# Kernel tuning notes

Measured on AMD Instinct MI355X. Metric: run time of the kernel, lower is better.

Reference implementation:

```python
import jax, jax.numpy as jnp
import numpy as np

B, H, W, C = 16, 64, 64, 512
WS, SS, NH = 8, 4, 16
HD = C // NH
N = WS * WS          # tokens per window = 64
NWH, NWW = H // WS, W // WS
NW = NWH * NWW       # windows per image = 64
HID = 2048
EPS = 1e-5

def _rel_pos_index():
    coords = np.stack(np.meshgrid(np.arange(WS), np.arange(WS), indexing='ij'))  # [2,ws,ws]
    cf = coords.reshape(2, -1)                      # [2,N]
    rel = cf[:, :, None] - cf[:, None, :]           # [2,N,N]
    rel = rel.transpose(1, 2, 0).astype(np.int64)   # [N,N,2]
    rel[:, :, 0] += WS - 1
    rel[:, :, 1] += WS - 1
    rel[:, :, 0] *= 2 * WS - 1
    return rel.sum(-1)                              # [N,N]

def _attn_mask():
    img = np.zeros((H, W), dtype=np.float32)
    cnt = 0
    sls = (slice(0, -WS), slice(-WS, -SS), slice(-SS, None))
    for hs in sls:
        for ws_ in sls:
            img[hs, ws_] = cnt
            cnt += 1
    mw = img.reshape(NWH, WS, NWW, WS).transpose(0, 2, 1, 3).reshape(-1, N)  # [nW,N]
    am = mw[:, None, :] - mw[:, :, None]            # [nW,N,N] (unsqueeze(1)-unsqueeze(2))
    return np.where(am != 0, np.float32(-100.0), np.float32(0.0))

_RPI = jnp.asarray(_rel_pos_index())
_AMASK = jnp.asarray(_attn_mask())

def _ln(x, g, b):
    m = jnp.mean(x, -1, keepdims=True)
    v = jnp.mean((x - m) ** 2, -1, keepdims=True)
    return (x - m) * jax.lax.rsqrt(v + EPS) * g + b

def setup_inputs() -> dict:
    key = jax.random.key(0)
    ks = jax.random.split(key, 8)
    s = 0.02
    return {
        'x': jax.random.normal(ks[0], (B, H * W, C), jnp.float32),
        'g1': jnp.ones((C,), jnp.float32), 'b1': jnp.zeros((C,), jnp.float32),
        'qkv_w': jax.random.normal(ks[1], (C, 3 * C), jnp.float32) * s,
        'qkv_b': jnp.zeros((3 * C,), jnp.float32),
        'proj_w': jax.random.normal(ks[2], (C, C), jnp.float32) * s,
        'proj_b': jnp.zeros((C,), jnp.float32),
        'rpb': jax.random.normal(ks[3], ((2 * WS - 1) ** 2, NH), jnp.float32) * s,
        'g2': jnp.ones((C,), jnp.float32), 'b2': jnp.zeros((C,), jnp.float32),
        'fc1_w': jax.random.normal(ks[4], (C, HID), jnp.float32) * s,
        'fc1_b': jnp.zeros((HID,), jnp.float32),
        'fc2_w': jax.random.normal(ks[5], (HID, C), jnp.float32) * s,
        'fc2_b': jnp.zeros((C,), jnp.float32),
    }

def reference(x, g1, b1, qkv_w, qkv_b, proj_w, proj_b, rpb, g2, b2, fc1_w, fc1_b, fc2_w, fc2_b):
    shortcut = x                                    # [B,L,C]
    xn = _ln(x, g1, b1).reshape(B, H, W, C)
    xs = jnp.roll(xn, (-SS, -SS), axis=(1, 2))      # cyclic shift
    # window partition -> [B*nW, N, C]
    xw = xs.reshape(B, NWH, WS, NWW, WS, C).transpose(0, 1, 3, 2, 4, 5).reshape(-1, N, C)
    # attention
    qkv = xw @ qkv_w + qkv_b                        # [Bw,N,3C]
    qkv = qkv.reshape(-1, N, 3, NH, HD).transpose(2, 0, 3, 1, 4)  # [3,Bw,NH,N,HD]
    q, k, v = qkv[0], qkv[1], qkv[2]
    scale = jnp.asarray(HD ** -0.5, xw.dtype)
    attn = jnp.einsum('bhnd,bhmd->bhnm', q, k) * scale            # [Bw,NH,N,N]
    bias = rpb[_RPI.reshape(-1)].reshape(N, N, NH).transpose(2, 0, 1)
    attn = attn + bias[None]
    attn = attn.reshape(B, NW, NH, N, N) + _AMASK[None, :, None]
    attn = jax.nn.softmax(attn.reshape(-1, NH, N, N), axis=-1)
    out = jnp.einsum('bhnm,bhmd->bhnd', attn, v)    # [Bw,NH,N,HD]
    out = out.transpose(0, 2, 1, 3).reshape(-1, N, C)
    out = out @ proj_w + proj_b
    # window reverse -> [B,H,W,C]
    xr = out.reshape(B, NWH, NWW, WS, WS, C).transpose(0, 1, 3, 2, 4, 5).reshape(B, H, W, C)
    xr = jnp.roll(xr, (SS, SS), axis=(1, 2)).reshape(B, H * W, C)
    x = shortcut + xr
    h = _ln(x, g2, b2)
    h = jax.nn.gelu(h @ fc1_w + fc1_b, approximate=False) @ fc2_w + fc2_b
    return x + h
```

## Files before the change

### kernel.cpp

```cpp
#include <hip/hip_runtime.h>
#include <hip/hip_bf16.h>

using f32x4  = __attribute__((ext_vector_type(4))) float;
using bf16x8 = __attribute__((ext_vector_type(8))) short;
using short8 = __attribute__((ext_vector_type(8))) short;
using s16x4  = __attribute__((ext_vector_type(4))) short;

#define DEVINL __device__ __forceinline__

DEVINL short f2bf(float f) {
  unsigned u = __builtin_bit_cast(unsigned, f);
  u += 0x7fffu + ((u >> 16) & 1u);
  return (short)(u >> 16);
}
DEVINL float bf2f(short h) {
  return __builtin_bit_cast(float, (unsigned)((unsigned short)h) << 16);
}

DEVINL float gelu_fast(float v) {
  float t = __expf(-1.5957691216057308f * (v + 0.044715f * v * v * v));
  return v * __builtin_amdgcn_rcpf(1.0f + t);
}

#define GLDS16(g, l) __builtin_amdgcn_global_load_lds( \
    (const __attribute__((address_space(1))) void*)(g), \
    (__attribute__((address_space(3))) void*)(l), 16, 0, 0)

__global__ __launch_bounds__(256)
void transpose_bf16(const float* __restrict__ in, short* __restrict__ out, int R, int C) {
  int idx = blockIdx.x * 256 + threadIdx.x;
  if (idx >= R * C) return;
  int c = idx / R, r = idx % R;
  out[idx] = f2bf(in[(size_t)r * C + c]);
}

__global__ __launch_bounds__(256)
void bias_expand(const float* __restrict__ rpb, float* __restrict__ BIASF) {
  int idx = blockIdx.x * 256 + threadIdx.x;
  int head = idx >> 12, n = (idx >> 6) & 63, m = idx & 63;
  int i1 = n >> 3, j1 = n & 7, i2 = m >> 3, j2 = m & 7;
  BIASF[idx] = rpb[((i1 - i2 + 7) * 15 + (j1 - j2 + 7)) * 16 + head];
}

template<int REMAP>
__global__ __launch_bounds__(256)
void ln_kernel(const float* __restrict__ X, const float* __restrict__ gamma,
               const float* __restrict__ beta, short* __restrict__ OUT) {
  const int lane = threadIdx.x & 63;
  const int wid  = threadIdx.x >> 6;
  const int t    = blockIdx.x * 4 + wid;
  const float* xp = X + (size_t)t * 512 + lane * 8;
  float4 a = *(const float4*)xp;
  float4 b = *(const float4*)(xp + 4);
  float s = a.x + a.y + a.z + a.w + b.x + b.y + b.z + b.w;
  float q = a.x*a.x + a.y*a.y + a.z*a.z + a.w*a.w
          + b.x*b.x + b.y*b.y + b.z*b.z + b.w*b.w;
#pragma unroll
  for (int d = 1; d < 64; d <<= 1) { s += __shfl_xor(s, d); q += __shfl_xor(q, d); }
  float mean = s * (1.0f / 512.0f);
  float var  = q * (1.0f / 512.0f) - mean * mean;
  float rstd = rsqrtf(var + 1e-5f);
  float4 g0 = *(const float4*)(gamma + lane * 8);
  float4 g1 = *(const float4*)(gamma + lane * 8 + 4);
  float4 b0 = *(const float4*)(beta + lane * 8);
  float4 b1 = *(const float4*)(beta + lane * 8 + 4);
  short8 o;
  o[0] = f2bf((a.x - mean) * rstd * g0.x + b0.x);
  o[1] = f2bf((a.y - mean) * rstd * g0.y + b0.y);
  o[2] = f2bf((a.z - mean) * rstd * g0.z + b0.z);
  o[3] = f2bf((a.w - mean) * rstd * g0.w + b0.w);
  o[4] = f2bf((b.x - mean) * rstd * g1.x + b1.x);
  o[5] = f2bf((b.y - mean) * rstd * g1.y + b1.y);
  o[6] = f2bf((b.z - mean) * rstd * g1.z + b1.z);
  o[7] = f2bf((b.w - mean) * rstd * g1.w + b1.w);
  size_t orow;
  if (REMAP) {
    int bb = t >> 12, l = t & 4095, hh = l >> 6, ww = l & 63;
    int hs = (hh + 60) & 63, ws2 = (ww + 60) & 63;
    orow = (size_t)(bb * 64 + (hs >> 3) * 8 + (ws2 >> 3)) * 64 + (hs & 7) * 8 + (ws2 & 7);
  } else {
    orow = (size_t)t;
  }
  *(short8*)(OUT + orow * 512 + lane * 8) = o;
}

__global__ __launch_bounds__(256)
void ln_bf16(const short* __restrict__ X, const float* __restrict__ gamma,
             const float* __restrict__ beta, short* __restrict__ OUT) {
  const int lane = threadIdx.x & 63;
  const int wid  = threadIdx.x >> 6;
  const int t    = blockIdx.x * 4 + wid;
  short8 v = *(const short8*)(X + (size_t)t * 512 + lane * 8);
  float f[8];
#pragma unroll
  for (int k = 0; k < 8; ++k) f[k] = bf2f(v[k]);
  float s = 0.f, q = 0.f;
#pragma unroll
  for (int k = 0; k < 8; ++k) { s += f[k]; q += f[k] * f[k]; }
#pragma unroll
  for (int d = 1; d < 64; d <<= 1) { s += __shfl_xor(s, d); q += __shfl_xor(q, d); }
  float mean = s * (1.0f / 512.0f);
  float var  = q * (1.0f / 512.0f) - mean * mean;
  float rstd = rsqrtf(var + 1e-5f);
  float4 g0 = *(const float4*)(gamma + lane * 8);
  float4 g1 = *(const float4*)(gamma + lane * 8 + 4);
  float4 b0 = *(const float4*)(beta + lane * 8);
  float4 b1 = *(const float4*)(beta + lane * 8 + 4);
  short8 o;
  o[0] = f2bf((f[0] - mean) * rstd * g0.x + b0.x);
  o[1] = f2bf((f[1] - mean) * rstd * g0.y + b0.y);
  o[2] = f2bf((f[2] - mean) * rstd * g0.z + b0.z);
  o[3] = f2bf((f[3] - mean) * rstd * g0.w + b0.w);
  o[4] = f2bf((f[4] - mean) * rstd * g1.x + b1.x);
  o[5] = f2bf((f[5] - mean) * rstd * g1.y + b1.y);
  o[6] = f2bf((f[6] - mean) * rstd * g1.z + b1.z);
  o[7] = f2bf((f[7] - mean) * rstd * g1.w + b1.w);
  *(short8*)(OUT + (size_t)t * 512 + lane * 8) = o;
}

__global__ __launch_bounds__(256)
void attn_core(const short* __restrict__ Q, const short* __restrict__ Kb,
               const short* __restrict__ VT, const float* __restrict__ BIASF,
               short* __restrict__ AOUT) {
  __shared__ short P[4][4096];
  const int tid = threadIdx.x, lane = tid & 63, wid = tid >> 6;
  const int lr = lane & 15, lg = lane >> 4;
  const int gw = blockIdx.x * 4 + wid;
  const int win = gw >> 4, head = gw & 15;
  const int wimg = win & 63, wh = wimg >> 3, ww = wimg & 7;
  const size_t qbase = (size_t)win * 64 * 512 + head * 32;
  short* Pb = P[wid];

  bf16x8 aq[4], bk[4];
#pragma unroll
  for (int tm = 0; tm < 4; ++tm) aq[tm] = *(const bf16x8*)(Q  + qbase + (size_t)(tm * 16 + lr) * 512 + lg * 8);
#pragma unroll
  for (int tn = 0; tn < 4; ++tn) bk[tn] = *(const bf16x8*)(Kb + qbase + (size_t)(tn * 16 + lr) * 512 + lg * 8);
  f32x4 sa[4][4] = {};
#pragma unroll
  for (int tm = 0; tm < 4; ++tm)
#pragma unroll
    for (int tn = 0; tn < 4; ++tn)
      sa[tm][tn] = __builtin_amdgcn_mfma_f32_16x16x32_bf16(aq[tm], bk[tn], sa[tm][tn], 0, 0, 0);

  const float* bias_h = BIASF + head * 4096;
  float inv[4][4];
#pragma unroll
  for (int tm = 0; tm < 4; ++tm) {
#pragma unroll
    for (int e = 0; e < 4; ++e) {
      const int n = tm * 16 + lg * 4 + e;
      const int i1 = n >> 3, j1 = n & 7;
      const int rh1 = (wh == 7) ? 1 + (i1 >> 2) : 0;
      const int rw1 = (ww == 7) ? 1 + (j1 >> 2) : 0;
      float v[4];
      float mx = -3.0e38f;
#pragma unroll
      for (int tn = 0; tn < 4; ++tn) {
        const int m = tn * 16 + lr;
        const int mi = (m >> 3), mj = m & 7;
        const int rh2 = (wh == 7) ? 1 + (mi >> 2) : 0;
        const int rw2 = (ww == 7) ? 1 + (mj >> 2) : 0;
        float val = sa[tm][tn][e] + bias_h[n * 64 + m]
                  + ((rh1 != rh2 || rw1 != rw2) ? -100.0f : 0.0f);
        v[tn] = val;
        mx = fmaxf(mx, val);
      }
#pragma unroll
      for (int d = 1; d < 16; d <<= 1) mx = fmaxf(mx, __shfl_xor(mx, d));
      float sum = 0.f;
#pragma unroll
      for (int tn = 0; tn < 4; ++tn) { v[tn] = __expf(v[tn] - mx); sum += v[tn]; }
#pragma unroll
      for (int d = 1; d < 16; d <<= 1) sum += __shfl_xor(sum, d);
      inv[tm][e] = 1.0f / sum;
      const int sw = (n & 7) << 3;
#pragma unroll
      for (int tn = 0; tn < 4; ++tn) Pb[n * 64 + ((tn * 16 + lr) ^ sw)] = f2bf(v[tn]);
    }
  }
  __syncthreads();

  f32x4 oa[4][2] = {};
  const short* vt = VT + (size_t)win * 32768 + head * 2048;
#pragma unroll
  for (int ks = 0; ks < 2; ++ks) {
    bf16x8 pa[4], bv[2];
#pragma unroll
    for (int tm = 0; tm < 4; ++tm) {
      const int r = tm * 16 + lr;
      pa[tm] = *(const bf16x8*)(Pb + r * 64 + ((ks * 32 + lg * 8) ^ ((r & 7) << 3)));
    }
#pragma unroll
    for (int t2 = 0; t2 < 2; ++t2) bv[t2] = *(const bf16x8*)(vt + (t2 * 16 + lr) * 64 + ks * 32 + lg * 8);
#pragma unroll
    for (int tm = 0; tm < 4; ++tm)
#pragma unroll
      for (int t2 = 0; t2 < 2; ++t2)
        oa[tm][t2] = __builtin_amdgcn_mfma_f32_16x16x32_bf16(pa[tm], bv[t2], oa[tm][t2], 0, 0, 0);
  }
#pragma unroll
  for (int tm = 0; tm < 4; ++tm)
#pragma unroll
    for (int t2 = 0; t2 < 2; ++t2)
#pragma unroll
      for (int e = 0; e < 4; ++e) {
        const int n = tm * 16 + lg * 4 + e;
        AOUT[((size_t)win * 64 + n) * 512 + head * 32 + t2 * 16 + lr] = f2bf(oa[tm][t2][e] * inv[tm][e]);
      }
}

template<int EPI, int K, int NX>
__global__ __launch_bounds__(512, 1)
void gemmBK64(const short* __restrict__ Aa, const short* __restrict__ Bb,
              const float* __restrict__ bias, const float* __restrict__ resid,
              const short* __restrict__ residh,
              float* __restrict__ outf, short* __restrict__ outh) {
  constexpr int NT = K / 64;
  __shared__ short L[24576];
  const int tid = threadIdx.x;
  const int lane = tid & 63, wid = tid >> 6;
  const int lr = lane & 15, lg = lane >> 4;
  const int wm = wid >> 1, wn = wid & 1;

  const int nwg = gridDim.x;
  const int id = blockIdx.x;
  const int id2 = (id & 7) * (nwg >> 3) + (id >> 3);
  const bool swapped = (EPI == 1 || EPI == 3);
  const int mt    = swapped ? (id2 % NX) : (id2 / NX);
  const int ntile = swapped ? (id2 / NX) : (id2 % NX);
  const int m0 = mt * 256, n0 = ntile * 128;

  const int rr = tid >> 3;
  const int ss = ((tid & 7) ^ (rr & 7)) * 8;
  const short* pA = Aa + (size_t)(m0 + rr) * K + ss;
  const short* pB = Bb + (size_t)(n0 + rr) * K + ss;
  char* Ld = (char*)L + tid * 16;

  const int xr = lr & 7;
  const char* rA0 = (char*)L + (wm * 64 + lr) * 128 + ((lg ^ xr) << 4);
  const char* rA1 = (char*)L + (wm * 64 + lr) * 128 + (((4 + lg) ^ xr) << 4);
  const char* rB0 = (char*)L + 32768 + (wn * 64 + lr) * 128 + ((lg ^ xr) << 4);
  const char* rB1 = (char*)L + 32768 + (wn * 64 + lr) * 128 + (((4 + lg) ^ xr) << 4);

  f32x4 acc[4][4] = {};
  for (int kt = 0; kt < NT; ++kt) {
    const int ko = kt * 64;
    GLDS16(pA + ko,                    Ld);
    GLDS16(pA + ko + (size_t)64  * K,  Ld + 8192);
    GLDS16(pA + ko + (size_t)128 * K,  Ld + 16384);
    GLDS16(pA + ko + (size_t)192 * K,  Ld + 24576);
    GLDS16(pB + ko,                    Ld + 32768);
    GLDS16(pB + ko + (size_t)64  * K,  Ld + 40960);
    __syncthreads();
    bf16x8 a[4], b[4];
#pragma unroll
    for (int i = 0; i < 4; ++i) a[i] = *(const bf16x8*)(rA0 + i * 2048);
#pragma unroll
    for (int j = 0; j < 4; ++j) b[j] = *(const bf16x8*)(rB0 + j * 2048);
#pragma unroll
    for (int i = 0; i < 4; ++i)
#pragma unroll
      for (int j = 0; j < 4; ++j)
        acc[i][j] = __builtin_amdgcn_mfma_f32_16x16x32_bf16(a[i], b[j], acc[i][j], 0, 0, 0);
#pragma unroll
    for (int i = 0; i < 4; ++i) a[i] = *(const bf16x8*)(rA1 + i * 2048);
#pragma unroll
    for (int j = 0; j < 4; ++j) b[j] = *(const bf16x8*)(rB1 + j * 2048);
#pragma unroll
    for (int i = 0; i < 4; ++i)
#pragma unroll
      for (int j = 0; j < 4; ++j)
        acc[i][j] = __builtin_amdgcn_mfma_f32_16x16x32_bf16(a[i], b[j], acc[i][j], 0, 0, 0);
    __syncthreads();
  }

  if (EPI == 1) {
#pragma unroll
    for (int i = 0; i < 4; ++i) {
      const int h0 = m0 + wm * 64 + i * 16 + lg * 4;
      const float4 bi = *(const float4*)(bias + h0);
#pragma unroll
      for (int j = 0; j < 4; ++j) {
        const int tok = n0 + wn * 64 + j * 16 + lr;
        s16x4 o;
        o[0] = f2bf(gelu_fast(acc[i][j][0] + bi.x));
        o[1] = f2bf(gelu_fast(acc[i][j][1] + bi.y));
        o[2] = f2bf(gelu_fast(acc[i][j][2] + bi.z));
        o[3] = f2bf(gelu_fast(acc[i][j][3] + bi.w));
        *(s16x4*)(outh + (size_t)tok * 2048 + h0) = o;
      }
    }
  } else if (EPI == 0) {
#pragma unroll
    for (int j = 0; j < 4; ++j) {
      const int col = n0 + wn * 64 + j * 16 + lr;
      const float bc = bias[col];
#pragma unroll
      for (int i = 0; i < 4; ++i)
#pragma unroll
        for (int e = 0; e < 4; ++e) {
          const int row = m0 + wm * 64 + i * 16 + lg * 4 + e;
          float v = acc[i][j][e] + bc;
          const int wv = row >> 6, n = row & 63;
          const int bb = wv >> 6, wi = wv & 63;
          const int hs = (wi >> 3) * 8 + (n >> 3), ws2 = (wi & 7) * 8 + (n & 7);
          const int hh = (hs + 4) & 63, wwp = (ws2 + 4) & 63;
          const size_t orow = (size_t)bb * 4096 + hh * 64 + wwp;
          outh[orow * 512 + col] = f2bf(resid[orow * 512 + col] + v);
        }
    }
  } else if (EPI == 2) {
#pragma unroll
    for (int j = 0; j < 4; ++j) {
      const int col = n0 + wn * 64 + j * 16 + lr;
      const float bc = bias[col];
#pragma unroll
      for (int i = 0; i < 4; ++i)
#pragma unroll
        for (int e = 0; e < 4; ++e) {
          const int row = m0 + wm * 64 + i * 16 + lg * 4 + e;
          outf[(size_t)row * 512 + col] = acc[i][j][e] + bc + bf2f(residh[(size_t)row * 512 + col]);
        }
    }
  } else {
    const int seg = m0 >> 9;
    const float qs = 0.17677669529663687f;
#pragma unroll
    for (int i = 0; i < 4; ++i) {
      const int oc0 = m0 + wm * 64 + i * 16 + lg * 4;
      const float4 bi = *(const float4*)(bias + oc0);
#pragma unroll
      for (int j = 0; j < 4; ++j) {
        const int tok = n0 + wn * 64 + j * 16 + lr;
        if (seg == 0) {
          s16x4 o;
          o[0] = f2bf((acc[i][j][0] + bi.x) * qs);
          o[1] = f2bf((acc[i][j][1] + bi.y) * qs);
          o[2] = f2bf((acc[i][j][2] + bi.z) * qs);
          o[3] = f2bf((acc[i][j][3] + bi.w) * qs);
          *(s16x4*)(outh + (size_t)tok * 512 + oc0) = o;
        } else if (seg == 1) {
          s16x4 o;
          o[0] = f2bf(acc[i][j][0] + bi.x);
          o[1] = f2bf(acc[i][j][1] + bi.y);
          o[2] = f2bf(acc[i][j][2] + bi.z);
          o[3] = f2bf(acc[i][j][3] + bi.w);
          *(s16x4*)(outh + 33554432 + (size_t)tok * 512 + (oc0 - 512)) = o;
        } else {
          const int cc0 = oc0 - 1024;
          short* vbase = outh + 67108864 +
              (size_t)((tok >> 6) * 16 + (cc0 >> 5)) * 2048 + (tok & 63);
          const int d0 = cc0 & 31;
          vbase[(d0 + 0) * 64] = f2bf(acc[i][j][0] + bi.x);
          vbase[(d0 + 1) * 64] = f2bf(acc[i][j][1] + bi.y);
          vbase[(d0 + 2) * 64] = f2bf(acc[i][j][2] + bi.z);
          vbase[(d0 + 3) * 64] = f2bf(acc[i][j][3] + bi.w);
        }
      }
    }
  }
}

extern "C" void kernel_launch(void* const* d_in, const int* in_sizes, int n_in,
                              void* d_out, int out_size, void* d_ws, size_t ws_size,
                              hipStream_t stream) {
  (void)in_sizes; (void)n_in; (void)out_size; (void)ws_size;
  const float* x      = (const float*)d_in[0];
  const float* g1     = (const float*)d_in[1];
  const float* b1     = (const float*)d_in[2];
  const float* qkv_w  = (const float*)d_in[3];
  const float* qkv_b  = (const float*)d_in[4];
  const float* proj_w = (const float*)d_in[5];
  const float* proj_b = (const float*)d_in[6];
  const float* rpb    = (const float*)d_in[7];
  const float* g2     = (const float*)d_in[8];
  const float* b2     = (const float*)d_in[9];
  const float* fc1_w  = (const float*)d_in[10];
  const float* fc1_b  = (const float*)d_in[11];
  const float* fc2_w  = (const float*)d_in[12];
  const float* fc2_b  = (const float*)d_in[13];
  float* out = (float*)d_out;
  char* ws = (char*)d_ws;

  short* WQKVT  = (short*)(ws);
  short* WPROJT = (short*)(ws + 1572864);
  short* WFC1T  = (short*)(ws + 2097152);
  short* WFC2T  = (short*)(ws + 4194304);
  short* X2B    = (short*)(ws + 6291456);
  float* BIASF  = (float*)(ws + 6291456);
  short* ATT    = (short*)(ws + 140509184);
  short* XW     = (short*)(ws + 207618048);
  short* QB     = (short*)(ws + 274726912);
  short* H1     = XW;
  short* X2N    = ATT;

  transpose_bf16<<<3072, 256, 0, stream>>>(qkv_w,  WQKVT, 512, 1536);
  transpose_bf16<<<1024, 256, 0, stream>>>(proj_w, WPROJT, 512, 512);
  transpose_bf16<<<4096, 256, 0, stream>>>(fc1_w,  WFC1T, 512, 2048);
  transpose_bf16<<<4096, 256, 0, stream>>>(fc2_w,  WFC2T, 2048, 512);
  bias_expand<<<256, 256, 0, stream>>>(rpb, BIASF);

  ln_kernel<1><<<16384, 256, 0, stream>>>(x, g1, b1, XW);
  gemmBK64<3, 512, 6><<<3072, 512, 0, stream>>>(WQKVT, XW, qkv_b, nullptr, nullptr, nullptr, QB);
  attn_core<<<4096, 256, 0, stream>>>(QB, QB + 33554432, QB + 67108864, BIASF, ATT);
  gemmBK64<0, 512, 4><<<1024, 512, 0, stream>>>(ATT, WPROJT, proj_b, x, nullptr, nullptr, X2B);
  ln_bf16<<<16384, 256, 0, stream>>>(X2B, g2, b2, X2N);
  gemmBK64<1, 512, 8><<<4096, 512, 0, stream>>>(WFC1T, X2N, fc1_b, nullptr, nullptr, nullptr, H1);
  gemmBK64<2, 2048, 4><<<1024, 512, 0, stream>>>(H1, WFC2T, fc2_b, nullptr, X2B, out, nullptr);
}
```

Before: 857.7 us.

## Pipeline GEMM mainloop with 4-stage BK32 LDS ring and async prefetch

Replaces the single-buffered BK64 GEMM mainloop, which synchronised twice per K step, with a 4-slot BK32 LDS ring. Global-to-LDS loads run three stages ahead, with explicit vmcnt waits and one barrier per phase. MFMA blocks are wrapped in raised wave priority so compute overlaps outstanding memory loads. This uses twice the LDS and hand-counted waitcnts, which is fragile if the compiler reorders memory operations.

```diff
diff --git a/kernel.cpp b/kernel.cpp
--- a/kernel.cpp
+++ b/kernel.cpp
@@ -25,6 +25,9 @@
 #define GLDS16(g, l) __builtin_amdgcn_global_load_lds( \
     (const __attribute__((address_space(1))) void*)(g), \
     (__attribute__((address_space(3))) void*)(l), 16, 0, 0)
+
+#define SBAR() __builtin_amdgcn_s_barrier()
+#define WAITV(n) asm volatile("s_waitcnt vmcnt(" #n ")" ::: "memory")
 
 __global__ __launch_bounds__(256)
 void transpose_bf16(const float* __restrict__ in, short* __restrict__ out, int R, int C) {
@@ -212,12 +215,12 @@
 
 template<int EPI, int K, int NX>
 __global__ __launch_bounds__(512, 1)
-void gemmBK64(const short* __restrict__ Aa, const short* __restrict__ Bb,
-              const float* __restrict__ bias, const float* __restrict__ resid,
-              const short* __restrict__ residh,
-              float* __restrict__ outf, short* __restrict__ outh) {
-  constexpr int NT = K / 64;
-  __shared__ short L[24576];
+void gemm8p(const short* __restrict__ Aa, const short* __restrict__ Bb,
+            const float* __restrict__ bias, const float* __restrict__ resid,
+            const short* __restrict__ residh,
+            float* __restrict__ outf, short* __restrict__ outh) {
+  constexpr int P = K / 32;
+  __shared__ short L[49152];
   const int tid = threadIdx.x;
   const int lane = tid & 63, wid = tid >> 6;
   const int lr = lane & 15, lg = lane >> 4;
@@ -231,49 +234,70 @@
   const int ntile = swapped ? (id2 / NX) : (id2 % NX);
   const int m0 = mt * 256, n0 = ntile * 128;
 
-  const int rr = tid >> 3;
-  const int ss = ((tid & 7) ^ (rr & 7)) * 8;
-  const short* pA = Aa + (size_t)(m0 + rr) * K + ss;
-  const short* pB = Bb + (size_t)(n0 + rr) * K + ss;
+  const int scol = (((tid & 3) ^ ((tid >> 3) & 3)) * 8);
+  const short* pA0 = Aa + (size_t)(m0 + (tid >> 2)) * K + scol;
+  const short* pA1 = Aa + (size_t)(m0 + 128 + (tid >> 2)) * K + scol;
+  const short* pB0 = Bb + (size_t)(n0 + (tid >> 2)) * K + scol;
   char* Ld = (char*)L + tid * 16;
 
-  const int xr = lr & 7;
-  const char* rA0 = (char*)L + (wm * 64 + lr) * 128 + ((lg ^ xr) << 4);
-  const char* rA1 = (char*)L + (wm * 64 + lr) * 128 + (((4 + lg) ^ xr) << 4);
-  const char* rB0 = (char*)L + 32768 + (wn * 64 + lr) * 128 + ((lg ^ xr) << 4);
-  const char* rB1 = (char*)L + 32768 + (wn * 64 + lr) * 128 + (((4 + lg) ^ xr) << 4);
+  auto stage = [&](int h) {
+    char* s = Ld + (h & 3) * 24576;
+    GLDS16(pA0 + h * 32, s);
+    GLDS16(pA1 + h * 32, s + 8192);
+    GLDS16(pB0 + h * 32, s + 16384);
+  };
+
+  const int xr2 = (lr >> 1) & 3;
+  const int rAoff = (wm * 64 + lr) * 64 + ((lg ^ xr2) << 4);
+  const int rBoff = 16384 + (wn * 64 + lr) * 64 + ((lg ^ xr2) << 4);
 
   f32x4 acc[4][4] = {};
-  for (int kt = 0; kt < NT; ++kt) {
-    const int ko = kt * 64;
-    GLDS16(pA + ko,                    Ld);
-    GLDS16(pA + ko + (size_t)64  * K,  Ld + 8192);
-    GLDS16(pA + ko + (size_t)128 * K,  Ld + 16384);
-    GLDS16(pA + ko + (size_t)192 * K,  Ld + 24576);
-    GLDS16(pB + ko,                    Ld + 32768);
-    GLDS16(pB + ko + (size_t)64  * K,  Ld + 40960);
-    __syncthreads();
-    bf16x8 a[4], b[4];
-#pragma unroll
-    for (int i = 0; i < 4; ++i) a[i] = *(const bf16x8*)(rA0 + i * 2048);
-#pragma unroll
-    for (int j = 0; j < 4; ++j) b[j] = *(const bf16x8*)(rB0 + j * 2048);
-#pragma unroll
-    for (int i = 0; i < 4; ++i)
-#pragma unroll
-      for (int j = 0; j < 4; ++j)
-        acc[i][j] = __builtin_amdgcn_mfma_f32_16x16x32_bf16(a[i], b[j], acc[i][j], 0, 0, 0);
-#pragma unroll
-    for (int i = 0; i < 4; ++i) a[i] = *(const bf16x8*)(rA1 + i * 2048);
-#pragma unroll
-    for (int j = 0; j < 4; ++j) b[j] = *(const bf16x8*)(rB1 + j * 2048);
-#pragma unroll
-    for (int i = 0; i < 4; ++i)
-#pragma unroll
-      for (int j = 0; j < 4; ++j)
-        acc[i][j] = __builtin_amdgcn_mfma_f32_16x16x32_bf16(a[i], b[j], acc[i][j], 0, 0, 0);
-    __syncthreads();
+  stage(0); stage(1); stage(2);
+  WAITV(6);
+  SBAR();
+  __builtin_amdgcn_sched_barrier(0);
+
+#define PHASE(S) do { \
+    const int h = p + (S); \
+    const char* Ls = (char*)L + (S) * 24576; \
+    bf16x8 a0 = *(const bf16x8*)(Ls + rAoff + 0 * 1024); \
+    bf16x8 a1 = *(const bf16x8*)(Ls + rAoff + 1 * 1024); \
+    bf16x8 a2 = *(const bf16x8*)(Ls + rAoff + 2 * 1024); \
+    bf16x8 a3 = *(const bf16x8*)(Ls + rAoff + 3 * 1024); \
+    bf16x8 b0 = *(const bf16x8*)(Ls + rBoff + 0 * 1024); \
+    bf16x8 b1 = *(const bf16x8*)(Ls + rBoff + 1 * 1024); \
+    bf16x8 b2 = *(const bf16x8*)(Ls + rBoff + 2 * 1024); \
+    bf16x8 b3 = *(const bf16x8*)(Ls + rBoff + 3 * 1024); \
+    if (h + 3 < P) stage(h + 3); \
+    __builtin_amdgcn_s_setprio(1); \
+    acc[0][0] = __builtin_amdgcn_mfma_f32_16x16x32_bf16(a0, b0, acc[0][0], 0, 0, 0); \
+    acc[0][1] = __builtin_amdgcn_mfma_f32_16x16x32_bf16(a0, b1, acc[0][1], 0, 0, 0); \
+    acc[0][2] = __builtin_amdgcn_mfma_f32_16x16x32_bf16(a0, b2, acc[0][2], 0, 0, 0); \
+    acc[0][3] = __builtin_amdgcn_mfma_f32_16x16x32_bf16(a0, b3, acc[0][3], 0, 0, 0); \
+    acc[1][0] = __builtin_amdgcn_mfma_f32_16x16x32_bf16(a1, b0, acc[1][0], 0, 0, 0); \
+    acc[1][1] = __builtin_amdgcn_mfma_f32_16x16x32_bf16(a1, b1, acc[1][1], 0, 0, 0); \
+    acc[1][2] = __builtin_amdgcn_mfma_f32_16x16x32_bf16(a1, b2, acc[1][2], 0, 0, 0); \
+    acc[1][3] = __builtin_amdgcn_mfma_f32_16x16x32_bf16(a1, b3, acc[1][3], 0, 0, 0); \
+    acc[2][0] = __builtin_amdgcn_mfma_f32_16x16x32_bf16(a2, b0, acc[2][0], 0, 0, 0); \
+    acc[2][1] = __builtin_amdgcn_mfma_f32_16x16x32_bf16(a2, b1, acc[2][1], 0, 0, 0); \
+    acc[2][2] = __builtin_amdgcn_mfma_f32_16x16x32_bf16(a2, b2, acc[2][2], 0, 0, 0); \
+    acc[2][3] = __builtin_amdgcn_mfma_f32_16x16x32_bf16(a2, b3, acc[2][3], 0, 0, 0); \
+    acc[3][0] = __builtin_amdgcn_mfma_f32_16x16x32_bf16(a3, b0, acc[3][0], 0, 0, 0); \
+    acc[3][1] = __builtin_amdgcn_mfma_f32_16x16x32_bf16(a3, b1, acc[3][1], 0, 0, 0); \
+    acc[3][2] = __builtin_amdgcn_mfma_f32_16x16x32_bf16(a3, b2, acc[3][2], 0, 0, 0); \
+    acc[3][3] = __builtin_amdgcn_mfma_f32_16x16x32_bf16(a3, b3, acc[3][3], 0, 0, 0); \
+    __builtin_amdgcn_s_setprio(0); \
+    if (h < P - 3)       { WAITV(6); } \
+    else if (h == P - 3) { WAITV(3); } \
+    else                 { WAITV(0); } \
+    SBAR(); \
+    __builtin_amdgcn_sched_barrier(0); \
+  } while (0)
+
+  for (int p = 0; p < P; p += 4) {
+    PHASE(0); PHASE(1); PHASE(2); PHASE(3);
   }
+#undef PHASE
 
   if (EPI == 1) {
 #pragma unroll
@@ -402,10 +426,10 @@
   bias_expand<<<256, 256, 0, stream>>>(rpb, BIASF);
 
   ln_kernel<1><<<16384, 256, 0, stream>>>(x, g1, b1, XW);
-  gemmBK64<3, 512, 6><<<3072, 512, 0, stream>>>(WQKVT, XW, qkv_b, nullptr, nullptr, nullptr, QB);
+  gemm8p<3, 512, 6><<<3072, 512, 0, stream>>>(WQKVT, XW, qkv_b, nullptr, nullptr, nullptr, QB);
   attn_core<<<4096, 256, 0, stream>>>(QB, QB + 33554432, QB + 67108864, BIASF, ATT);
-  gemmBK64<0, 512, 4><<<1024, 512, 0, stream>>>(ATT, WPROJT, proj_b, x, nullptr, nullptr, X2B);
+  gemm8p<0, 512, 4><<<1024, 512, 0, stream>>>(ATT, WPROJT, proj_b, x, nullptr, nullptr, X2B);
   ln_bf16<<<16384, 256, 0, stream>>>(X2B, g2, b2, X2N);
-  gemmBK64<1, 512, 8><<<4096, 512, 0, stream>>>(WFC1T, X2N, fc1_b, nullptr, nullptr, nullptr, H1);
-  gemmBK64<2, 2048, 4><<<1024, 512, 0, stream>>>(H1, WFC2T, fc2_b, nullptr, X2B, out, nullptr);
-}
+  gemm8p<1, 512, 8><<<4096, 512, 0, stream>>>(WFC1T, X2N, fc1_b, nullptr, nullptr, nullptr, H1);
+  gemm8p<2, 2048, 4><<<1024, 512, 0, stream>>>(H1, WFC2T, fc2_b, nullptr, X2B, out, nullptr);
+}
```

After: 854.7 us. Within noise of the previous version (-0.4%).
